# Kernel optimization log

Hardware: AMD Instinct MI355X
Metric: run time of the kernel (lower is better)

The kernel has to match this reference:

```python
import jax, jax.numpy as jnp
import numpy as np


def grid_sample_3d(vol, grid, align_corners=False):
    """PyTorch-equivalent 5D grid_sample, trilinear, padding_mode='zeros'.
    vol: [N,C,D,H,W]; grid: [N,Do,Ho,Wo,3] with last dim (x,y,z) in normalized coords.
    """
    N, C, D, H, W = vol.shape

    def unnorm(c, s):
        s = jnp.asarray(s, vol.dtype)
        if align_corners:
            return (c + 1.0) * (s - 1.0) * 0.5
        return ((c + 1.0) * s - 1.0) * 0.5

    ix = unnorm(grid[..., 0], W)  # [N,Do,Ho,Wo]
    iy = unnorm(grid[..., 1], H)
    iz = unnorm(grid[..., 2], D)

    def sample_one(vn, ix, iy, iz):
        # vn: [C,D,H,W]; ix/iy/iz: [Do,Ho,Wo]
        x0 = jnp.floor(ix); y0 = jnp.floor(iy); z0 = jnp.floor(iz)
        tx = ix - x0; ty = iy - y0; tz = iz - z0

        def corner(dz, dy, dx):
            zc = z0 + dz; yc = y0 + dy; xc = x0 + dx
            w = (tz if dz else 1.0 - tz) * (ty if dy else 1.0 - ty) * (tx if dx else 1.0 - tx)
            inb = (zc >= 0) & (zc < D) & (yc >= 0) & (yc < H) & (xc >= 0) & (xc < W)
            zi = jnp.clip(zc, 0, D - 1).astype(jnp.int32)
            yi = jnp.clip(yc, 0, H - 1).astype(jnp.int32)
            xi = jnp.clip(xc, 0, W - 1).astype(jnp.int32)
            v = vn[:, zi, yi, xi]  # [C,Do,Ho,Wo]
            return v * (w * inb.astype(vn.dtype))[None]

        acc = corner(0, 0, 0)
        for dz in (0, 1):
            for dy in (0, 1):
                for dx in (0, 1):
                    if (dz, dy, dx) != (0, 0, 0):
                        acc = acc + corner(dz, dy, dx)
        return acc

    return jax.vmap(sample_one)(vol, ix, iy, iz)


def _to_sample_grid(locs_chfirst):
    # [N,3,D,H,W] channel order (z_idx,y_idx,x_idx) -> [N,D,H,W,3] (x,y,z)
    return jnp.moveaxis(locs_chfirst, 1, -1)[..., ::-1]


def setup_inputs() -> dict:
    key = jax.random.key(0)
    k0, k1, k2 = jax.random.split(key, 3)
    D, H, W = 160, 192, 160
    src = jax.random.normal(k0, (1, 1, D, H, W), jnp.float32)
    flow1 = jax.random.normal(k1, (1, 3, D, H, W), jnp.float32) * 5.0
    flow2 = jax.random.normal(k2, (1, 3, D, H, W), jnp.float32) * 5.0
    vs = [jnp.arange(s, dtype=jnp.float32) for s in (D, H, W)]
    grid = jnp.stack(jnp.meshgrid(*vs, indexing='ij'))[None]  # [1,3,D,H,W]
    range_flow = jnp.float32(0.4)
    return {"src": src, "flow1": flow1, "flow2": flow2, "grid": grid, "range_flow": range_flow}


def reference(src, flow1, flow2, grid, range_flow):
    D, H, W = flow1.shape[2:]
    # normalization 2*(c/(s-1)-0.5) per spatial channel (align_corners=True convention,
    # but grid_sample is called with torch's default align_corners=False -> replicate)
    scales = jnp.array([D - 1, H - 1, W - 1], jnp.float32).reshape(1, 3, 1, 1, 1)

    # (deform_1_img from flow1 alone is computed in the original but never returned)

    # warp flow1 by flow2 -- NOTE: the original passes UNNORMALIZED voxel coords here
    grid2 = grid + flow2 * range_flow  # [1,3,D,H,W]
    flow1_warped = grid_sample_3d(flow1, _to_sample_grid(grid2), align_corners=False)
    out_flow = flow1_warped + flow2

    new_locs_total = grid + out_flow * range_flow
    new_locs_total = 2.0 * (new_locs_total / scales - 0.5)
    deform_2_img = grid_sample_3d(src, _to_sample_grid(new_locs_total), align_corners=False)
    return (deform_2_img, out_flow)
```

## Files before the change

### kernel.cpp

```cpp
#include <hip/hip_runtime.h>

#define DD 160
#define HH 192
#define WW 160
constexpr int DHW = DD * HH * WW;

typedef float vfloat4 __attribute__((ext_vector_type(4)));
typedef float vfloat2 __attribute__((ext_vector_type(2)));

__device__ __forceinline__ vfloat2 load_pair(const float* __restrict__ p) {
    vfloat2 r;
    __builtin_memcpy(&r, p, 8);
    return r;
}

__global__ __launch_bounds__(256) void st_fused_kernel(
    const float* __restrict__ src,
    const float* __restrict__ flow1,
    const float* __restrict__ flow2,
    const float* __restrict__ prf,
    float* __restrict__ out)
{
    int bid = (int)blockIdx.x;
    int nb  = (int)gridDim.x;
    int swz = bid;
    if ((nb & 7) == 0) {
        int chunk = nb >> 3;
        swz = (bid & 7) * chunk + (bid >> 3);
    }
    int tid  = swz * 256 + (int)threadIdx.x;
    int idx0 = tid * 4;
    if (idx0 >= DHW) return;

    const float rf = prf[0];

    int xb = idx0 % WW;
    int t  = idx0 / WW;
    int y  = t % HH;
    int z  = t / HH;

    const vfloat4 f2zv = __builtin_nontemporal_load((const vfloat4*)(flow2 + idx0));
    const vfloat4 f2yv = __builtin_nontemporal_load((const vfloat4*)(flow2 + idx0 + DHW));
    const vfloat4 f2xv = __builtin_nontemporal_load((const vfloat4*)(flow2 + idx0 + 2 * DHW));

    float fwz[4], fwy[4], fwx[4];
    #pragma unroll
    for (int j = 0; j < 4; ++j) {
        fwz[j] = 0.0f; fwy[j] = 0.0f; fwx[j] = 0.0f;
        int x = xb + j;
        float g2z = (float)z + f2zv[j] * rf;
        float g2y = (float)y + f2yv[j] * rf;
        float g2x = (float)x + f2xv[j] * rf;
        float iz = ((g2z + 1.0f) * (float)DD - 1.0f) * 0.5f;
        float iy = ((g2y + 1.0f) * (float)HH - 1.0f) * 0.5f;
        float ix = ((g2x + 1.0f) * (float)WW - 1.0f) * 0.5f;
        if (ix > -1.0f && ix < (float)WW &&
            iy > -1.0f && iy < (float)HH &&
            iz > -1.0f && iz < (float)DD) {
            float zf = floorf(iz), yf = floorf(iy), xf = floorf(ix);
            int z0 = (int)zf, y0 = (int)yf, x0 = (int)xf;
            float tz = iz - zf, ty = iy - yf, tx = ix - xf;
            #pragma unroll
            for (int dz = 0; dz < 2; ++dz) {
                int zc = z0 + dz;
                if (zc < 0 || zc >= DD) continue;
                float wzc = dz ? tz : 1.0f - tz;
                #pragma unroll
                for (int dy = 0; dy < 2; ++dy) {
                    int yc = y0 + dy;
                    if (yc < 0 || yc >= HH) continue;
                    float wzy = wzc * (dy ? ty : 1.0f - ty);
                    #pragma unroll
                    for (int dx = 0; dx < 2; ++dx) {
                        int xc = x0 + dx;
                        if (xc < 0 || xc >= WW) continue;
                        float w = wzy * (dx ? tx : 1.0f - tx);
                        int off = (zc * HH + yc) * WW + xc;
                        fwz[j] += w * flow1[off];
                        fwy[j] += w * flow1[off + DHW];
                        fwx[j] += w * flow1[off + 2 * DHW];
                    }
                }
            }
        }
    }

    vfloat4 vofz, vofy, vofx;
    float wzw[4][2], wyw[4][2];
    float wxa[4], wxb[4];
    int   off[4][2][2];

    #pragma unroll
    for (int j = 0; j < 4; ++j) {
        int x = xb + j;
        float ofz = fwz[j] + f2zv[j];
        float ofy = fwy[j] + f2yv[j];
        float ofx = fwx[j] + f2xv[j];
        vofz[j] = ofz; vofy[j] = ofy; vofx[j] = ofx;

        float nz = (float)z + ofz * rf;
        float ny = (float)y + ofy * rf;
        float nx = (float)x + ofx * rf;
        float cz = 2.0f * (nz / (float)(DD - 1) - 0.5f);
        float cy = 2.0f * (ny / (float)(HH - 1) - 0.5f);
        float cx = 2.0f * (nx / (float)(WW - 1) - 0.5f);
        float sz2 = ((cz + 1.0f) * (float)DD - 1.0f) * 0.5f;
        float sy2 = ((cy + 1.0f) * (float)HH - 1.0f) * 0.5f;
        float sx2 = ((cx + 1.0f) * (float)WW - 1.0f) * 0.5f;

        float zf = floorf(sz2), yf = floorf(sy2), xf = floorf(sx2);
        int z0 = (int)zf, y0 = (int)yf, x0 = (int)xf;
        float tz = sz2 - zf, ty = sy2 - yf, tx = sx2 - xf;

        float wzp[2] = {1.0f - tz, tz};
        float wyp[2] = {1.0f - ty, ty};
        int zi[2], yi[2];
        #pragma unroll
        for (int d = 0; d < 2; ++d) {
            int zc = z0 + d, yc = y0 + d;
            if (zc < 0 || zc >= DD) wzp[d] = 0.0f;
            if (yc < 0 || yc >= HH) wyp[d] = 0.0f;
            zi[d] = min(max(zc, 0), DD - 1);
            yi[d] = min(max(yc, 0), HH - 1);
        }
        wzw[j][0] = wzp[0]; wzw[j][1] = wzp[1];
        wyw[j][0] = wyp[0]; wyw[j][1] = wyp[1];

        float wx0 = 1.0f - tx, wx1 = tx;
        if (x0 < 0 || x0 >= WW)          wx0 = 0.0f;
        if (x0 + 1 < 0 || x0 + 1 >= WW)  wx1 = 0.0f;
        bool lo = (x0 < 0);
        bool hi = (x0 > WW - 2);
        int xbase = min(max(x0, 0), WW - 2);
        wxa[j] = lo ? wx1 : (hi ? 0.0f : wx0);
        wxb[j] = hi ? wx0 : (lo ? 0.0f : wx1);

        #pragma unroll
        for (int dz = 0; dz < 2; ++dz)
            #pragma unroll
            for (int dy = 0; dy < 2; ++dy)
                off[j][dz][dy] = (zi[dz] * HH + yi[dy]) * WW + xbase;
    }

    vfloat2 v[4][4];
    #pragma unroll
    for (int j = 0; j < 4; ++j)
        #pragma unroll
        for (int dz = 0; dz < 2; ++dz)
            #pragma unroll
            for (int dy = 0; dy < 2; ++dy)
                v[j][dz * 2 + dy] = load_pair(src + off[j][dz][dy]);

    vfloat4 sval;
    #pragma unroll
    for (int j = 0; j < 4; ++j) {
        float acc = 0.0f;
        #pragma unroll
        for (int dz = 0; dz < 2; ++dz)
            #pragma unroll
            for (int dy = 0; dy < 2; ++dy) {
                float wzy = wzw[j][dz] * wyw[j][dy];
                vfloat2 p = v[j][dz * 2 + dy];
                acc = fmaf(wzy, fmaf(wxa[j], p.x, wxb[j] * p.y), acc);
            }
        sval[j] = acc;
    }

    __builtin_nontemporal_store(sval, (vfloat4*)(out + idx0));
    __builtin_nontemporal_store(vofz, (vfloat4*)(out + DHW + idx0));
    __builtin_nontemporal_store(vofy, (vfloat4*)(out + 2 * DHW + idx0));
    __builtin_nontemporal_store(vofx, (vfloat4*)(out + 3 * DHW + idx0));
}

extern "C" void kernel_launch(void* const* d_in, const int* in_sizes, int n_in,
                              void* d_out, int out_size, void* d_ws, size_t ws_size,
                              hipStream_t stream) {
    const float* src   = (const float*)d_in[0];
    const float* flow1 = (const float*)d_in[1];
    const float* flow2 = (const float*)d_in[2];
    const float* prf   = (const float*)d_in[4];
    float* out = (float*)d_out;

    int threads_total = DHW / 4;
    int blocks = (threads_total + 255) / 256;
    st_fused_kernel<<<blocks, 256, 0, stream>>>(src, flow1, flow2, prf, out);
}
```

Measured before the change: 252.5 us.

## Stage src halo tile in LDS for second trilinear sample, retile blocks to 3D

Blocks now cover an 8x16x16 3D tile with 512 threads and cooperatively load a padded src region (the tile plus a 6/5/5 halo) into shared memory. Second-stage samples whose 2x2x2 footprint falls inside that region read from LDS; the rest fall back to global loads. The aim is to replace scattered global gathers of src with on-chip reuse, since the displacements are small. In exchange each block loads about 25x27x27 floats, adds a __syncthreads, and uses more LDS, which may reduce occupancy.

```diff
diff --git a/kernel.cpp b/kernel.cpp
--- a/kernel.cpp
+++ b/kernel.cpp
@@ -4,6 +4,22 @@
 #define HH 192
 #define WW 160
 constexpr int DHW = DD * HH * WW;
+
+#define TZ 8
+#define TY 16
+#define TX 16
+#define HZ 6
+#define HY 5
+#define HX 5
+#define RZ (TZ + 2*HZ + 1)
+#define RY (TY + 2*HY + 1)
+#define RX (TX + 2*HX + 1)
+constexpr int RYX = RY * RX;
+constexpr int RE  = RZ * RYX;
+
+#define NBX (WW / TX)
+#define NBY (HH / TY)
+#define NBZ (DD / TZ)
 
 typedef float vfloat4 __attribute__((ext_vector_type(4)));
 typedef float vfloat2 __attribute__((ext_vector_type(2)));
@@ -14,34 +30,53 @@
     return r;
 }
 
-__global__ __launch_bounds__(256) void st_fused_kernel(
+__global__ __launch_bounds__(512) void st_fused_kernel(
     const float* __restrict__ src,
     const float* __restrict__ flow1,
     const float* __restrict__ flow2,
     const float* __restrict__ prf,
     float* __restrict__ out)
 {
-    int bid = (int)blockIdx.x;
-    int nb  = (int)gridDim.x;
-    int swz = bid;
-    if ((nb & 7) == 0) {
-        int chunk = nb >> 3;
-        swz = (bid & 7) * chunk + (bid >> 3);
-    }
-    int tid  = swz * 256 + (int)threadIdx.x;
-    int idx0 = tid * 4;
-    if (idx0 >= DHW) return;
+    __shared__ float sm[RE];
+
+    int bid   = (int)blockIdx.x;
+    int chunk = (int)gridDim.x >> 3;
+    int swz   = (bid & 7) * chunk + (bid >> 3);
+
+    int bx = swz % NBX;
+    int by = (swz / NBX) % NBY;
+    int bz = swz / (NBX * NBY);
+
+    int t  = (int)threadIdx.x;
+    int xg = t & 3;
+    int lyt = (t >> 2) & 15;
+    int lzt = t >> 6;
+
+    int xb = bx * TX + xg * 4;
+    int y  = by * TY + lyt;
+    int z  = bz * TZ + lzt;
+    int idx0 = (z * HH + y) * WW + xb;
 
     const float rf = prf[0];
-
-    int xb = idx0 % WW;
-    int t  = idx0 / WW;
-    int y  = t % HH;
-    int z  = t / HH;
 
     const vfloat4 f2zv = __builtin_nontemporal_load((const vfloat4*)(flow2 + idx0));
     const vfloat4 f2yv = __builtin_nontemporal_load((const vfloat4*)(flow2 + idx0 + DHW));
     const vfloat4 f2xv = __builtin_nontemporal_load((const vfloat4*)(flow2 + idx0 + 2 * DHW));
+
+    int gz0 = bz * TZ - HZ;
+    int gy0 = by * TY - HY;
+    int gx0 = bx * TX - HX;
+    for (int i = t; i < RE; i += 512) {
+        int rz  = i / RYX;
+        int rem = i - rz * RYX;
+        int ry  = rem / RX;
+        int rx  = rem - ry * RX;
+        int gz = min(max(gz0 + rz, 0), DD - 1);
+        int gy = min(max(gy0 + ry, 0), HH - 1);
+        int gx = min(max(gx0 + rx, 0), WW - 1);
+        sm[i] = src[(gz * HH + gy) * WW + gx];
+    }
+    __syncthreads();
 
     float fwz[4], fwy[4], fwx[4];
     #pragma unroll
@@ -85,11 +120,7 @@
         }
     }
 
-    vfloat4 vofz, vofy, vofx;
-    float wzw[4][2], wyw[4][2];
-    float wxa[4], wxb[4];
-    int   off[4][2][2];
-
+    vfloat4 sval, vofz, vofy, vofx;
     #pragma unroll
     for (int j = 0; j < 4; ++j) {
         int x = xb + j;
@@ -112,57 +143,48 @@
         int z0 = (int)zf, y0 = (int)yf, x0 = (int)xf;
         float tz = sz2 - zf, ty = sy2 - yf, tx = sx2 - xf;
 
-        float wzp[2] = {1.0f - tz, tz};
-        float wyp[2] = {1.0f - ty, ty};
-        int zi[2], yi[2];
-        #pragma unroll
-        for (int d = 0; d < 2; ++d) {
-            int zc = z0 + d, yc = y0 + d;
-            if (zc < 0 || zc >= DD) wzp[d] = 0.0f;
-            if (yc < 0 || yc >= HH) wyp[d] = 0.0f;
-            zi[d] = min(max(zc, 0), DD - 1);
-            yi[d] = min(max(yc, 0), HH - 1);
+        float wz0 = 1.0f - tz, wz1 = tz;
+        float wy0 = 1.0f - ty, wy1 = ty;
+        float wx0 = 1.0f - tx, wx1 = tx;
+        if (z0 < 0     || z0 >= DD)     wz0 = 0.0f;
+        if (z0 + 1 < 0 || z0 + 1 >= DD) wz1 = 0.0f;
+        if (y0 < 0     || y0 >= HH)     wy0 = 0.0f;
+        if (y0 + 1 < 0 || y0 + 1 >= HH) wy1 = 0.0f;
+        if (x0 < 0     || x0 >= WW)     wx0 = 0.0f;
+        if (x0 + 1 < 0 || x0 + 1 >= WW) wx1 = 0.0f;
+
+        int lxi = x0 - gx0, lyi = y0 - gy0, lzi = z0 - gz0;
+        bool inreg = ((unsigned)lxi <= (unsigned)(RX - 2)) &&
+                     ((unsigned)lyi <= (unsigned)(RY - 2)) &&
+                     ((unsigned)lzi <= (unsigned)(RZ - 2));
+
+        float acc;
+        if (inreg) {
+            int b = lzi * RYX + lyi * RX + lxi;
+            float r00 = fmaf(wx0, sm[b],             wx1 * sm[b + 1]);
+            float r01 = fmaf(wx0, sm[b + RX],        wx1 * sm[b + RX + 1]);
+            float r10 = fmaf(wx0, sm[b + RYX],       wx1 * sm[b + RYX + 1]);
+            float r11 = fmaf(wx0, sm[b + RYX + RX],  wx1 * sm[b + RYX + RX + 1]);
+            acc = wz0 * fmaf(wy0, r00, wy1 * r01)
+                + wz1 * fmaf(wy0, r10, wy1 * r11);
+        } else {
+            int zi0 = min(max(z0, 0), DD - 1), zi1 = min(max(z0 + 1, 0), DD - 1);
+            int yi0 = min(max(y0, 0), HH - 1), yi1 = min(max(y0 + 1, 0), HH - 1);
+            bool lo = (x0 < 0), hi = (x0 > WW - 2);
+            int xbase = min(max(x0, 0), WW - 2);
+            float wxa = lo ? wx1 : (hi ? 0.0f : wx0);
+            float wxb = hi ? wx0 : (lo ? 0.0f : wx1);
+            vfloat2 p00 = load_pair(src + (zi0 * HH + yi0) * WW + xbase);
+            vfloat2 p01 = load_pair(src + (zi0 * HH + yi1) * WW + xbase);
+            vfloat2 p10 = load_pair(src + (zi1 * HH + yi0) * WW + xbase);
+            vfloat2 p11 = load_pair(src + (zi1 * HH + yi1) * WW + xbase);
+            float r00 = fmaf(wxa, p00.x, wxb * p00.y);
+            float r01 = fmaf(wxa, p01.x, wxb * p01.y);
+            float r10 = fmaf(wxa, p10.x, wxb * p10.y);
+            float r11 = fmaf(wxa, p11.x, wxb * p11.y);
+            acc = wz0 * fmaf(wy0, r00, wy1 * r01)
+                + wz1 * fmaf(wy0, r10, wy1 * r11);
         }
-        wzw[j][0] = wzp[0]; wzw[j][1] = wzp[1];
-        wyw[j][0] = wyp[0]; wyw[j][1] = wyp[1];
-
-        float wx0 = 1.0f - tx, wx1 = tx;
-        if (x0 < 0 || x0 >= WW)          wx0 = 0.0f;
-        if (x0 + 1 < 0 || x0 + 1 >= WW)  wx1 = 0.0f;
-        bool lo = (x0 < 0);
-        bool hi = (x0 > WW - 2);
-        int xbase = min(max(x0, 0), WW - 2);
-        wxa[j] = lo ? wx1 : (hi ? 0.0f : wx0);
-        wxb[j] = hi ? wx0 : (lo ? 0.0f : wx1);
-
-        #pragma unroll
-        for (int dz = 0; dz < 2; ++dz)
-            #pragma unroll
-            for (int dy = 0; dy < 2; ++dy)
-                off[j][dz][dy] = (zi[dz] * HH + yi[dy]) * WW + xbase;
-    }
-
-    vfloat2 v[4][4];
-    #pragma unroll
-    for (int j = 0; j < 4; ++j)
-        #pragma unroll
-        for (int dz = 0; dz < 2; ++dz)
-            #pragma unroll
-            for (int dy = 0; dy < 2; ++dy)
-                v[j][dz * 2 + dy] = load_pair(src + off[j][dz][dy]);
-
-    vfloat4 sval;
-    #pragma unroll
-    for (int j = 0; j < 4; ++j) {
-        float acc = 0.0f;
-        #pragma unroll
-        for (int dz = 0; dz < 2; ++dz)
-            #pragma unroll
-            for (int dy = 0; dy < 2; ++dy) {
-                float wzy = wzw[j][dz] * wyw[j][dy];
-                vfloat2 p = v[j][dz * 2 + dy];
-                acc = fmaf(wzy, fmaf(wxa[j], p.x, wxb[j] * p.y), acc);
-            }
         sval[j] = acc;
     }
 
@@ -181,7 +203,6 @@
     const float* prf   = (const float*)d_in[4];
     float* out = (float*)d_out;
 
-    int threads_total = DHW / 4;
-    int blocks = (threads_total + 255) / 256;
-    st_fused_kernel<<<blocks, 256, 0, stream>>>(src, flow1, flow2, prf, out);
+    int blocks = NBX * NBY * NBZ;
+    st_fused_kernel<<<blocks, 512, 0, stream>>>(src, flow1, flow2, prf, out);
 }
```

Result: slower. 268.6 us (+6.4%).
